# Performance work log

Measured on AMD Instinct MI355X. Metric: run time of the kernel, lower is better.

The kernel has to match this reference:

```python
import jax, jax.numpy as jnp
import numpy as np

B, N, K = 64, 4096, 16
DIN, DOUT, HID, T = 256, 256, 512, 3
LN_EPS = 1e-5


def _ln2d(x, w, b):
    # LayerNorm over last TWO dims (matches nn.LayerNorm([n_feat, dim]))
    m = jnp.mean(x, axis=(-2, -1), keepdims=True)
    v = jnp.mean(jnp.square(x - m), axis=(-2, -1), keepdims=True)
    return (x - m) * jax.lax.rsqrt(v + LN_EPS) * w + b


def setup_inputs() -> dict:
    key = jax.random.key(0)
    ks = jax.random.split(key, 24)
    s = lambda fan_in: 1.0 / np.sqrt(fan_in)
    d = {
        "inputs": jax.random.normal(ks[0], (B, N, DIN), jnp.float32),
        "slots_init": jax.random.normal(ks[1], (B, K, DOUT), jnp.float32),
        "mu": jax.random.normal(ks[2], (1, 1, DOUT), jnp.float32),
        "logsigma": jax.random.normal(ks[3], (1, 1, DOUT), jnp.float32) * 0.1,
        "ln0_w": jnp.ones((N, DIN), jnp.float32),
        "ln0_b": jnp.zeros((N, DIN), jnp.float32),
        "ln1_w": jnp.ones((K, DOUT), jnp.float32),
        "ln1_b": jnp.zeros((K, DOUT), jnp.float32),
        "ln2_w": jnp.ones((K, DOUT), jnp.float32),
        "ln2_b": jnp.zeros((K, DOUT), jnp.float32),
        "qW": jax.random.uniform(ks[4], (T, DOUT, DOUT), jnp.float32, -s(DOUT), s(DOUT)),
        "qb": jax.random.uniform(ks[5], (T, DOUT), jnp.float32, -s(DOUT), s(DOUT)),
        "kW": jax.random.uniform(ks[6], (T, DOUT, DIN), jnp.float32, -s(DIN), s(DIN)),
        "kb": jax.random.uniform(ks[7], (T, DOUT), jnp.float32, -s(DIN), s(DIN)),
        "vW": jax.random.uniform(ks[8], (T, DOUT, DIN), jnp.float32, -s(DIN), s(DIN)),
        "vb": jax.random.uniform(ks[9], (T, DOUT), jnp.float32, -s(DIN), s(DIN)),
        "m1W": jax.random.uniform(ks[10], (T, HID, DOUT), jnp.float32, -s(DOUT), s(DOUT)),
        "m1b": jax.random.uniform(ks[11], (T, HID), jnp.float32, -s(DOUT), s(DOUT)),
        "m2W": jax.random.uniform(ks[12], (T, DOUT, HID), jnp.float32, -s(HID), s(HID)),
        "m2b": jax.random.uniform(ks[13], (T, DOUT), jnp.float32, -s(HID), s(HID)),
    }
    return d


def reference(inputs, slots_init, mu, logsigma, ln0_w, ln0_b, ln1_w, ln1_b,
              ln2_w, ln2_b, qW, qb, kW, kb, vW, vb, m1W, m1b, m2W, m2b):
    slots = mu + jnp.exp(logsigma) * slots_init          # [B,K,DOUT]
    x = _ln2d(inputs, ln0_w, ln0_b)                      # [B,N,DIN]
    for it in range(T):
        s = _ln2d(slots, ln1_w, ln1_b)
        q = jnp.einsum('bkd,ed->bke', s, qW[it]) + qb[it]     # [B,K,DOUT]
        k = jnp.einsum('bnd,ed->bne', x, kW[it]) + kb[it]     # [B,N,DOUT]
        v = jnp.einsum('bnd,ed->bne', x, vW[it]) + vb[it]     # [B,N,DOUT]
        dist = jnp.einsum('bkd,bnd->bkn', q, k) / K           # note: /out_num_features
        attns = jax.nn.softmax(dist, axis=1)                  # softmax over SLOT dim
        weights = attns / (jnp.sum(attns, axis=-1, keepdims=True) + 1e-7)
        slots = jnp.einsum('bkn,bnd->bkd', weights, v)        # [B,K,DOUT]
        h = _ln2d(slots, ln2_w, ln2_b)
        h = jax.nn.relu(jnp.einsum('bkd,hd->bkh', h, m1W[it]) + m1b[it])
        slots = slots + jnp.einsum('bkh,dh->bkd', h, m2W[it]) + m2b[it]
    return slots
```

## Files before the change

kernel.cpp:

```cpp
#include <hip/hip_runtime.h>
#include <hip/hip_bf16.h>

#define LN_EPS 1e-5f

typedef __attribute__((ext_vector_type(8))) short short8;
typedef __attribute__((ext_vector_type(4))) float f32x4;

__device__ __forceinline__ ushort f2bf(float f) {
    __hip_bfloat16 h = __float2bfloat16(f);
    return *reinterpret_cast<ushort*>(&h);
}
__device__ __forceinline__ float bf2f(ushort u) {
    union { float f; unsigned int i; } c; c.i = ((unsigned int)u) << 16; return c.f;
}

__global__ void kprep(const float* __restrict__ qW, const float* __restrict__ kW,
                      const float* __restrict__ m1W, const float* __restrict__ m2W,
                      const float* __restrict__ vW,
                      ushort* __restrict__ qWc, ushort* __restrict__ kWT,
                      ushort* __restrict__ m1Wc, ushort* __restrict__ m2Wc,
                      ushort* __restrict__ vWc,
                      const float* __restrict__ inp, float* __restrict__ sums) {
    __shared__ float tile[64][65];
    __shared__ float r1[256], r2[256];
    int blk = blockIdx.x, t = threadIdx.x;
    if (blk < 288) {
        int col = t & 63, rq = t >> 6;
        const float* src; ushort* dst; int C, tr, tc;
        if (blk < 48)        { int it = blk >> 4, rem = blk & 15; C = 256; tr = rem >> 2; tc = rem & 3;
                               src = qW + it * 65536;  dst = qWc + it * 65536; }
        else if (blk < 96)   { int li = blk - 48; int it = li >> 4, rem = li & 15; C = 256; tr = rem >> 2; tc = rem & 3;
                               src = vW + it * 65536;  dst = vWc + it * 65536; }
        else if (blk < 192)  { int li = blk - 96; int it = li >> 5, rem = li & 31; C = 256; tr = rem >> 2; tc = rem & 3;
                               src = m1W + it * 131072; dst = m1Wc + it * 131072; }
        else                 { int li = blk - 192; int it = li >> 5, rem = li & 31; C = 512; tr = rem >> 3; tc = rem & 7;
                               src = m2W + it * 131072; dst = m2Wc + it * 131072; }
        #pragma unroll
        for (int r = 0; r < 16; r++) {
            int row = r * 4 + rq;
            int idx = (tr * 64 + row) * C + tc * 64 + col;
            dst[idx] = f2bf(src[idx]);
        }
        return;
    }
    if (blk < 336) {
        int col = t & 63, rq = t >> 6;
        int li = blk - 288; int it = li >> 4, rem = li & 15;
        int tr = rem >> 2, tc = rem & 3;
        const float* src = kW + it * 65536; ushort* dst = kWT + it * 65536;
        #pragma unroll
        for (int r = 0; r < 16; r++) {
            int row = r * 4 + rq;
            tile[row][col] = src[(tr * 64 + row) * 256 + tc * 64 + col];
        }
        __syncthreads();
        #pragma unroll
        for (int r = 0; r < 16; r++) {
            int row = r * 4 + rq;
            dst[(tc * 64 + row) * 256 + tr * 64 + col] = f2bf(tile[col][row]);
        }
        return;
    }
    int lb = blk - 336;
    int b = lb >> 5, seg = lb & 31;
    const float4* p = (const float4*)inp + (size_t)b * 262144 + seg * 8192 + t;
    float s = 0.f, sq = 0.f;
    #pragma unroll
    for (int k = 0; k < 32; k++) {
        float4 v = p[k * 256];
        s  += v.x + v.y + v.z + v.w;
        sq += v.x * v.x + v.y * v.y + v.z * v.z + v.w * v.w;
    }
    r1[t] = s; r2[t] = sq; __syncthreads();
    for (int st = 128; st > 0; st >>= 1) {
        if (t < st) { r1[t] += r1[t + st]; r2[t] += r2[t + st]; }
        __syncthreads();
    }
    if (t == 0) { atomicAdd(&sums[b], r1[0]); atomicAdd(&sums[64 + b], r2[0]); }
}

__device__ __forceinline__ void qgen_core(
        int b, int t, int lane, int w, int l15, int quad,
        ushort* slbq, float* qsf, ushort* qsb, ushort* qkl,
        const ushort* __restrict__ qWc, const float* __restrict__ qb,
        const ushort* __restrict__ kWT, const float* __restrict__ kb,
        ushort* __restrict__ qkf, float* __restrict__ qkb,
        float* __restrict__ denom_out) {
    {
        short8 aq[8];
        #pragma unroll
        for (int ds = 0; ds < 8; ds++)
            aq[ds] = *(const short8*)(&slbq[l15 * 264 + ds * 32 + quad * 8]);
        int et = w;
        f32x4 c = f32x4{0.f, 0.f, 0.f, 0.f};
        #pragma unroll
        for (int ds = 0; ds < 8; ds++) {
            short8 bf_ = *(const short8*)(qWc + (size_t)(et * 16 + l15) * 256 + ds * 32 + quad * 8);
            c = __builtin_amdgcn_mfma_f32_16x16x32_bf16(aq[ds], bf_, c, 0, 0, 0);
        }
        float qbv = qb[et * 16 + l15];
        #pragma unroll
        for (int r = 0; r < 4; r++) {
            float val = (c[r] + qbv) * (1.f / 16.f);
            qsf[(quad * 4 + r) * 260 + et * 16 + l15] = val;
            qsb[(quad * 4 + r) * 264 + et * 16 + l15] = f2bf(val);
        }
    }
    __syncthreads();
    {
        float pp = 0.f;
        #pragma unroll
        for (int e = 0; e < 16; e++) pp += qsf[w * 260 + l15 * 16 + e] * kb[l15 * 16 + e];
        pp += __shfl_xor(pp, 1); pp += __shfl_xor(pp, 2);
        pp += __shfl_xor(pp, 4); pp += __shfl_xor(pp, 8);
        if (lane == 0) qkb[b * 16 + w] = pp;
    }
    if (t < 16) denom_out[b * 16 + t] = 0.f;
    {
        short8 aq2[8];
        #pragma unroll
        for (int es = 0; es < 8; es++)
            aq2[es] = *(const short8*)(&qsb[l15 * 264 + es * 32 + quad * 8]);
        int dt = w;
        f32x4 c2 = f32x4{0.f, 0.f, 0.f, 0.f};
        #pragma unroll
        for (int es = 0; es < 8; es++) {
            short8 bf2 = *(const short8*)(kWT + (size_t)(dt * 16 + l15) * 256 + es * 32 + quad * 8);
            c2 = __builtin_amdgcn_mfma_f32_16x16x32_bf16(aq2[es], bf2, c2, 0, 0, 0);
        }
        #pragma unroll
        for (int r = 0; r < 4; r++)
            qkl[(quad * 4 + r) * 264 + dt * 16 + l15] = f2bf(c2[r]);
    }
    __syncthreads();
    if (w < 8) {
        short8 v = *(const short8*)(&qkl[l15 * 264 + w * 32 + quad * 8]);
        *(short8*)(qkf + (size_t)(b * 8 + w) * 512 + lane * 8) = v;
    }
}

__global__ void lkq(const float* __restrict__ inp, const float* __restrict__ ln0w,
                    const float* __restrict__ ln0b, const float* __restrict__ sums,
                    ushort* __restrict__ xgs,
                    const float* __restrict__ slots_init, const float* __restrict__ mu,
                    const float* __restrict__ logsig,
                    const float* __restrict__ ln1w, const float* __restrict__ ln1b,
                    const ushort* __restrict__ qWc, const float* __restrict__ qb,
                    const ushort* __restrict__ kWT, const float* __restrict__ kb,
                    ushort* __restrict__ qkf, float* __restrict__ qkb,
                    float* __restrict__ denom) {
    __shared__ ushort slbq[16 * 264];
    __shared__ ushort qsb[16 * 264];
    __shared__ ushort qkl[16 * 264];
    __shared__ float  qsf[16 * 260];
    __shared__ float  wr1[16], wr2[16];
    int t = threadIdx.x;
    int lane = t & 63, w = t >> 6, l15 = lane & 15, quad = lane >> 4;

    if (blockIdx.x < 256) {
        int gw = blockIdx.x * 16 + w;
        int ntile = gw >> 4;
        int ds = (gw >> 1) & 7;
        int b0 = (gw & 1) * 32;
        int n = ntile * 16 + l15;
        int dcol = ds * 32 + quad * 8;
        const float4* wp = (const float4*)(ln0w + n * 256 + dcol);
        const float4* bp = (const float4*)(ln0b + n * 256 + dcol);
        float4 w0 = wp[0], w1 = wp[1];
        float4 c0 = bp[0], c1 = bp[1];
        #pragma unroll 4
        for (int bi = 0; bi < 32; bi++) {
            int b = b0 + bi;
            float mean = sums[b] * (1.f / 1048576.f);
            float rstd = rsqrtf(sums[64 + b] * (1.f / 1048576.f) - mean * mean + LN_EPS);
            const float4* xp = (const float4*)(inp + (size_t)b * 1048576 + n * 256 + dcol);
            float4 v0 = xp[0], v1 = xp[1];
            ushort o[8];
            o[0] = f2bf((v0.x - mean) * rstd * w0.x + c0.x);
            o[1] = f2bf((v0.y - mean) * rstd * w0.y + c0.y);
            o[2] = f2bf((v0.z - mean) * rstd * w0.z + c0.z);
            o[3] = f2bf((v0.w - mean) * rstd * w0.w + c0.w);
            o[4] = f2bf((v1.x - mean) * rstd * w1.x + c1.x);
            o[5] = f2bf((v1.y - mean) * rstd * w1.y + c1.y);
            o[6] = f2bf((v1.z - mean) * rstd * w1.z + c1.z);
            o[7] = f2bf((v1.w - mean) * rstd * w1.w + c1.w);
            *(short8*)(xgs + ((size_t)((b * 256 + ntile) * 8 + ds) * 64 + lane) * 8) = *(short8*)o;
        }
        return;
    }
    int b = blockIdx.x - 256;
    int g = t >> 8, c = t & 255;
    float muv = mu[c];
    float sgv = __expf(logsig[c]);
    float vals[4]; float s = 0.f, sq = 0.f;
    #pragma unroll
    for (int kk = 0; kk < 4; kk++) {
        float v = muv + sgv * slots_init[b * 4096 + (g * 4 + kk) * 256 + c];
        vals[kk] = v; s += v; sq += v * v;
    }
    #pragma unroll
    for (int m = 1; m < 64; m <<= 1) { s += __shfl_xor(s, m); sq += __shfl_xor(sq, m); }
    if (lane == 0) { wr1[w] = s; wr2[w] = sq; }
    __syncthreads();
    float ts = 0.f, tsq = 0.f;
    #pragma unroll
    for (int i = 0; i < 16; i++) { ts += wr1[i]; tsq += wr2[i]; }
    float m_  = ts * (1.f / 4096.f);
    float rs_ = rsqrtf(tsq * (1.f / 4096.f) - m_ * m_ + LN_EPS);
    #pragma unroll
    for (int kk = 0; kk < 4; kk++) {
        int k = g * 4 + kk;
        slbq[k * 264 + c] = f2bf((vals[kk] - m_) * rs_ * ln1w[k * 256 + c] + ln1b[k * 256 + c]);
    }
    __syncthreads();
    qgen_core(b, t, lane, w, l15, quad, slbq, qsf, qsb, qkl,
              qWc, qb, kWT, kb, qkf, qkb, denom);
}

__launch_bounds__(256, 4)
__global__ void katt(const ushort* __restrict__ xgs, const ushort* __restrict__ qkf,
                     const float* __restrict__ qkb, float* __restrict__ denom,
                     float* __restrict__ partials) {
    int b = blockIdx.x >> 4, chunk = blockIdx.x & 15;
    int tid = threadIdx.x;
    int lane = tid & 63, w = tid >> 6;
    int l15 = lane & 15, quad = lane >> 4;

    __shared__ ushort xtT[16384];
    __shared__ ushort attn[16 * 72];

    short8 ilo, ihi;
    #pragma unroll
    for (int j = 0; j < 8; j++) {
        ilo[j] = (short)((quad * 8 + j == l15)      ? 0x3F80 : 0);
        ihi[j] = (short)((quad * 8 + j == l15 + 16) ? 0x3F80 : 0);
    }
    int wbase = (w >> 1) * 512 + ((w * 2 + (quad >> 1)) & 3) * 128 + l15 * 8 + (quad & 1) * 4;

    short8 qkfr[8];
    #pragma unroll
    for (int ds = 0; ds < 8; ds++)
        qkfr[ds] = *(const short8*)(qkf + ((size_t)(b * 8 + ds) * 512 + lane * 8));
    float4 qo = *(const float4*)(qkb + b * 16 + quad * 4);

    f32x4 pacc[4];
    #pragma unroll
    for (int u = 0; u < 4; u++) pacc[u] = f32x4{0.f, 0.f, 0.f, 0.f};
    float dp0 = 0.f, dp1 = 0.f, dp2 = 0.f, dp3 = 0.f;

    int tile0 = b * 256 + chunk * 16;

    short8 pf[8];
    #pragma unroll
    for (int i = 0; i < 8; i++)
        pf[i] = *(const short8*)(xgs + (((size_t)(tile0 + w) * 8 + i) * 64 + lane) * 8);

    #pragma unroll 1
    for (int sub = 0; sub < 4; sub++) {
        __syncthreads();
        f32x4 dc = f32x4{0.f, 0.f, 0.f, 0.f};
        #pragma unroll
        for (int ds = 0; ds < 8; ds++)
            dc = __builtin_amdgcn_mfma_f32_16x16x32_bf16(qkfr[ds], pf[ds], dc, 0, 0, 0);
        dc[0] += qo.x; dc[1] += qo.y; dc[2] += qo.z; dc[3] += qo.w;
        float mx = fmaxf(fmaxf(dc[0], dc[1]), fmaxf(dc[2], dc[3]));
        mx = fmaxf(mx, __shfl_xor(mx, 16));
        mx = fmaxf(mx, __shfl_xor(mx, 32));
        float e0 = __expf(dc[0] - mx), e1 = __expf(dc[1] - mx);
        float e2 = __expf(dc[2] - mx), e3 = __expf(dc[3] - mx);
        float lsum = e0 + e1 + e2 + e3;
        lsum += __shfl_xor(lsum, 16); lsum += __shfl_xor(lsum, 32);
        float inv = 1.f / lsum;
        float p0 = e0 * inv, p1 = e1 * inv, p2 = e2 * inv, p3 = e3 * inv;
        dp0 += p0; dp1 += p1; dp2 += p2; dp3 += p3;
        attn[(quad * 4 + 0) * 72 + w * 16 + l15] = f2bf(p0);
        attn[(quad * 4 + 1) * 72 + w * 16 + l15] = f2bf(p1);
        attn[(quad * 4 + 2) * 72 + w * 16 + l15] = f2bf(p2);
        attn[(quad * 4 + 3) * 72 + w * 16 + l15] = f2bf(p3);
        f32x4 zz = f32x4{0.f, 0.f, 0.f, 0.f};
        #pragma unroll
        for (int ds = 0; ds < 8; ds++) {
            f32x4 tlo = __builtin_amdgcn_mfma_f32_16x16x32_bf16(pf[ds], ilo, zz, 0, 0, 0);
            f32x4 thi = __builtin_amdgcn_mfma_f32_16x16x32_bf16(pf[ds], ihi, zz, 0, 0, 0);
            unsigned lo0 = (__float_as_uint(tlo[0]) >> 16) | (__float_as_uint(tlo[1]) & 0xFFFF0000u);
            unsigned lo1 = (__float_as_uint(tlo[2]) >> 16) | (__float_as_uint(tlo[3]) & 0xFFFF0000u);
            unsigned hi0 = (__float_as_uint(thi[0]) >> 16) | (__float_as_uint(thi[1]) & 0xFFFF0000u);
            unsigned hi1 = (__float_as_uint(thi[2]) >> 16) | (__float_as_uint(thi[3]) & 0xFFFF0000u);
            *(uint2*)(&xtT[(ds * 2 + 0) * 1024 + wbase]) = make_uint2(lo0, lo1);
            *(uint2*)(&xtT[(ds * 2 + 1) * 1024 + wbase]) = make_uint2(hi0, hi1);
        }
        if (sub < 3) {
            #pragma unroll
            for (int i = 0; i < 8; i++)
                pf[i] = *(const short8*)(xgs + (((size_t)(tile0 + (sub + 1) * 4 + w) * 8 + i) * 64 + lane) * 8);
        }
        __syncthreads();

        #pragma unroll
        for (int ns = 0; ns < 2; ns++) {
            short8 aa = *(const short8*)(&attn[l15 * 72 + ns * 32 + quad * 8]);
            #pragma unroll
            for (int u = 0; u < 4; u++) {
                short8 bb = *(const short8*)(&xtT[((w * 4 + u) * 2 + ns) * 512 + lane * 8]);
                pacc[u] = __builtin_amdgcn_mfma_f32_16x16x32_bf16(aa, bb, pacc[u], 0, 0, 0);
            }
        }
    }

    #pragma unroll
    for (int m = 1; m < 16; m <<= 1) {
        dp0 += __shfl_xor(dp0, m); dp1 += __shfl_xor(dp1, m);
        dp2 += __shfl_xor(dp2, m); dp3 += __shfl_xor(dp3, m);
    }
    if (l15 == 0) {
        atomicAdd(&denom[b * 16 + quad * 4 + 0], dp0);
        atomicAdd(&denom[b * 16 + quad * 4 + 1], dp1);
        atomicAdd(&denom[b * 16 + quad * 4 + 2], dp2);
        atomicAdd(&denom[b * 16 + quad * 4 + 3], dp3);
    }

    float* pout = partials + (size_t)(b * 16 + chunk) * 4096;
    #pragma unroll
    for (int u = 0; u < 4; u++)
        #pragma unroll
        for (int r = 0; r < 4; r++)
            pout[(quad * 4 + r) * 256 + (w * 4 + u) * 16 + l15] = pacc[u][r];
}

__global__ void ktail(const float* __restrict__ partials, const float* __restrict__ denom,
                      const ushort* __restrict__ vWc, const float* __restrict__ vb,
                      const float* __restrict__ ln2w, const float* __restrict__ ln2b,
                      const ushort* __restrict__ m1Wc, const float* __restrict__ m1b,
                      const ushort* __restrict__ m2Wc, const float* __restrict__ m2b,
                      float* __restrict__ final_out, int write_final,
                      const float* __restrict__ ln1w, const float* __restrict__ ln1b,
                      const ushort* __restrict__ qWc_n, const float* __restrict__ qb_n,
                      const ushort* __restrict__ kWT_n, const float* __restrict__ kb_n,
                      ushort* __restrict__ qkf, float* __restrict__ qkb,
                      float* __restrict__ denom_out, int gen) {
    int b = blockIdx.x, t = threadIdx.x;
    int lane = t & 63, w = t >> 6, l15 = lane & 15, quad = lane >> 4;

    __shared__ char pool[60416];
    __shared__ float dnb[16];
    __shared__ float wr1[16], wr2[16];
    ushort* axsb = (ushort*)pool;
    ushort* s2b  = (ushort*)(pool + 8448);
    float*  slt  = (float*)(pool + 16896);
    ushort* hlb  = (ushort*)(pool + 35328);
    float*  slt2 = (float*)pool;
    ushort* slbq = (ushort*)(pool + 16896);
    ushort* qkl  = (ushort*)(pool + 16896);
    float*  qsf  = (float*)(pool + 35328);
    ushort* qsb  = (ushort*)(pool + 51968);

    const float* pp = partials + (size_t)b * 65536;
    #pragma unroll
    for (int i = 0; i < 4; i++) {
        int idx = i * 1024 + t;
        float ss = 0.f;
        #pragma unroll
        for (int c = 0; c < 16; c++) ss += pp[c * 4096 + idx];
        axsb[(idx >> 8) * 264 + (idx & 255)] = f2bf(ss);
    }
    if (t < 16) dnb[t] = denom[b * 16 + t];
    __syncthreads();

    float myv[4];
    {
        short8 af[8];
        #pragma unroll
        for (int ds = 0; ds < 8; ds++)
            af[ds] = *(const short8*)(&axsb[l15 * 264 + ds * 32 + quad * 8]);
        int et = w;
        f32x4 c = f32x4{0.f, 0.f, 0.f, 0.f};
        #pragma unroll
        for (int ds = 0; ds < 8; ds++) {
            short8 bf_ = *(const short8*)(vWc + (size_t)(et * 16 + l15) * 256 + ds * 32 + quad * 8);
            c = __builtin_amdgcn_mfma_f32_16x16x32_bf16(af[ds], bf_, c, 0, 0, 0);
        }
        float vbe = vb[et * 16 + l15];
        #pragma unroll
        for (int r = 0; r < 4; r++) {
            float A = dnb[quad * 4 + r];
            float val = (c[r] + vbe * A) / (A + 1e-7f);
            slt[(quad * 4 + r) * 256 + et * 16 + l15] = val;
            myv[r] = val;
        }
    }
    {
        float s = myv[0] + myv[1] + myv[2] + myv[3];
        float sq = myv[0]*myv[0] + myv[1]*myv[1] + myv[2]*myv[2] + myv[3]*myv[3];
        #pragma unroll
        for (int m = 1; m < 64; m <<= 1) { s += __shfl_xor(s, m); sq += __shfl_xor(sq, m); }
        if (lane == 0) { wr1[w] = s; wr2[w] = sq; }
        __syncthreads();
    }
    float ts = 0.f, tsq = 0.f;
    #pragma unroll
    for (int i = 0; i < 16; i++) { ts += wr1[i]; tsq += wr2[i]; }
    float m2_ = ts * (1.f / 4096.f);
    float rs2 = rsqrtf(tsq * (1.f / 4096.f) - m2_ * m2_ + LN_EPS);
    {
        int e = w * 16 + l15;
        #pragma unroll
        for (int r = 0; r < 4; r++) {
            int ss_ = quad * 4 + r;
            s2b[ss_ * 264 + e] = f2bf((myv[r] - m2_) * rs2 * ln2w[ss_ * 256 + e] + ln2b[ss_ * 256 + e]);
        }
    }
    __syncthreads();

    {
        short8 a2[8];
        #pragma unroll
        for (int ds = 0; ds < 8; ds++)
            a2[ds] = *(const short8*)(&s2b[l15 * 264 + ds * 32 + quad * 8]);
        #pragma unroll
        for (int p = 0; p < 2; p++) {
            int jt = w + p * 16;
            f32x4 c = f32x4{0.f, 0.f, 0.f, 0.f};
            #pragma unroll
            for (int ds = 0; ds < 8; ds++) {
                short8 bf_ = *(const short8*)(m1Wc + (size_t)(jt * 16 + l15) * 256 + ds * 32 + quad * 8);
                c = __builtin_amdgcn_mfma_f32_16x16x32_bf16(a2[ds], bf_, c, 0, 0, 0);
            }
            float bias = m1b[jt * 16 + l15];
            #pragma unroll
            for (int r = 0; r < 4; r++)
                hlb[(quad * 4 + r) * 520 + jt * 16 + l15] = f2bf(fmaxf(c[r] + bias, 0.f));
        }
    }
    __syncthreads();

    {
        short8 a3[16];
        #pragma unroll
        for (int js = 0; js < 16; js++)
            a3[js] = *(const short8*)(&hlb[l15 * 520 + js * 32 + quad * 8]);
        int dt = w;
        f32x4 c = f32x4{0.f, 0.f, 0.f, 0.f};
        #pragma unroll
        for (int js = 0; js < 16; js++) {
            short8 bf_ = *(const short8*)(m2Wc + (size_t)(dt * 16 + l15) * 512 + js * 32 + quad * 8);
            c = __builtin_amdgcn_mfma_f32_16x16x32_bf16(a3[js], bf_, c, 0, 0, 0);
        }
        float b2 = m2b[dt * 16 + l15];
        #pragma unroll
        for (int r = 0; r < 4; r++) {
            int ss_ = quad * 4 + r, d = dt * 16 + l15;
            float val = slt[ss_ * 256 + d] + c[r] + b2;
            slt2[ss_ * 256 + d] = val;
            if (write_final) final_out[(size_t)b * 4096 + ss_ * 256 + d] = val;
        }
    }
    __syncthreads();

    if (gen) {
        int g = t >> 8, cc = t & 255;
        float vals[4]; float s = 0.f, sq = 0.f;
        #pragma unroll
        for (int kk = 0; kk < 4; kk++) {
            float v = slt2[(g * 4 + kk) * 256 + cc];
            vals[kk] = v; s += v; sq += v * v;
        }
        #pragma unroll
        for (int m = 1; m < 64; m <<= 1) { s += __shfl_xor(s, m); sq += __shfl_xor(sq, m); }
        if (lane == 0) { wr1[w] = s; wr2[w] = sq; }
        __syncthreads();
        float ts1 = 0.f, tsq1 = 0.f;
        #pragma unroll
        for (int i = 0; i < 16; i++) { ts1 += wr1[i]; tsq1 += wr2[i]; }
        float m1_ = ts1 * (1.f / 4096.f);
        float rs1 = rsqrtf(tsq1 * (1.f / 4096.f) - m1_ * m1_ + LN_EPS);
        #pragma unroll
        for (int kk = 0; kk < 4; kk++) {
            int k = g * 4 + kk;
            slbq[k * 264 + cc] = f2bf((vals[kk] - m1_) * rs1 * ln1w[k * 256 + cc] + ln1b[k * 256 + cc]);
        }
        __syncthreads();
        qgen_core(b, t, lane, w, l15, quad, slbq, qsf, qsb, qkl,
                  qWc_n, qb_n, kWT_n, kb_n, qkf, qkb, denom_out);
    }
}

extern "C" void kernel_launch(void* const* d_in, const int* in_sizes, int n_in,
                              void* d_out, int out_size, void* d_ws, size_t ws_size,
                              hipStream_t stream) {
    const float* inputs     = (const float*)d_in[0];
    const float* slots_init = (const float*)d_in[1];
    const float* mu         = (const float*)d_in[2];
    const float* logsig     = (const float*)d_in[3];
    const float* ln0w       = (const float*)d_in[4];
    const float* ln0b       = (const float*)d_in[5];
    const float* ln1w       = (const float*)d_in[6];
    const float* ln1b       = (const float*)d_in[7];
    const float* ln2w       = (const float*)d_in[8];
    const float* ln2b       = (const float*)d_in[9];
    const float* qW         = (const float*)d_in[10];
    const float* qb         = (const float*)d_in[11];
    const float* kW         = (const float*)d_in[12];
    const float* kb         = (const float*)d_in[13];
    const float* vW         = (const float*)d_in[14];
    const float* vb         = (const float*)d_in[15];
    const float* m1W        = (const float*)d_in[16];
    const float* m1b        = (const float*)d_in[17];
    const float* m2W        = (const float*)d_in[18];
    const float* m2b        = (const float*)d_in[19];

    char* ws = (char*)d_ws;
    ushort* xgs     = (ushort*)(ws);
    float*  partials= (float*)(ws + 134217728);
    ushort* qkf     = (ushort*)(ws + 150994944);
    ushort* qWc     = (ushort*)(ws + 153616384);
    ushort* m1Wc    = (ushort*)(ws + 154009600);
    ushort* m2Wc    = (ushort*)(ws + 154796032);
    ushort* vWc     = (ushort*)(ws + 155582464);
    float*  denom   = (float*)(ws + 155975680);
    float*  qkb     = (float*)(ws + 155979776);
    float*  sums    = (float*)(ws + 155983872);
    ushort* kWT     = (ushort*)(ws + 155984384);

    hipMemsetAsync(sums, 0, 512, stream);
    kprep<<<2384, 256, 0, stream>>>(qW, kW, m1W, m2W, vW, qWc, kWT, m1Wc, m2Wc, vWc,
                                    inputs, sums);
    lkq<<<320, 1024, 0, stream>>>(inputs, ln0w, ln0b, sums, xgs,
                                  slots_init, mu, logsig, ln1w, ln1b,
                                  qWc, qb, kWT, kb, qkf, qkb, denom);

    for (int it = 0; it < 3; it++) {
        katt<<<1024, 256, 0, stream>>>(xgs, qkf, qkb, denom, partials);
        int nx = (it < 2) ? it + 1 : 2;
        ktail<<<64, 1024, 0, stream>>>(partials, denom,
                                       vWc + it * 65536, vb + it * 256, ln2w, ln2b,
                                       m1Wc + it * 131072, m1b + it * 512,
                                       m2Wc + it * 131072, m2b + it * 256,
                                       (float*)d_out, it == 2 ? 1 : 0,
                                       ln1w, ln1b,
                                       qWc + nx * 65536, qb + nx * 256,
                                       kWT + nx * 65536, kb + nx * 256,
                                       qkf, qkb, denom, it < 2 ? 1 : 0);
    }
}
```

Before: 316.9 us.

## Fuse tail into attention kernel via last-block-per-batch atomic counter

Removes the separate ktail launch by having each attention block increment a per-batch counter. The last of the 16 chunk blocks for a batch then runs the tail work: reduce the partials, apply the V projection, LayerNorm, the MLP, and generate the next iteration's q/k. This cuts a kernel launch and its grid-wide barrier per iteration. The cost is that the tail now runs on only 256 threads instead of 1024 and adds threadfence/atomic overhead, so the last block per batch can lengthen the critical path.

```diff
diff --git a/kernel.cpp b/kernel.cpp
--- a/kernel.cpp
+++ b/kernel.cpp
@@ -218,16 +218,28 @@
 }
 
 __launch_bounds__(256, 4)
-__global__ void katt(const ushort* __restrict__ xgs, const ushort* __restrict__ qkf,
-                     const float* __restrict__ qkb, float* __restrict__ denom,
-                     float* __restrict__ partials) {
+__global__ void katta(const ushort* __restrict__ xgs, ushort* __restrict__ qkf,
+                      float* __restrict__ qkb, float* __restrict__ denom,
+                      float* __restrict__ partials, int* __restrict__ cnt,
+                      const ushort* __restrict__ vWc, const float* __restrict__ vb,
+                      const float* __restrict__ ln2w, const float* __restrict__ ln2b,
+                      const ushort* __restrict__ m1Wc, const float* __restrict__ m1b,
+                      const ushort* __restrict__ m2Wc, const float* __restrict__ m2b,
+                      float* __restrict__ final_out, int write_final,
+                      const float* __restrict__ ln1w, const float* __restrict__ ln1b,
+                      const ushort* __restrict__ qWc_n, const float* __restrict__ qb_n,
+                      const ushort* __restrict__ kWT_n, const float* __restrict__ kb_n,
+                      int gen) {
     int b = blockIdx.x >> 4, chunk = blockIdx.x & 15;
     int tid = threadIdx.x;
     int lane = tid & 63, w = tid >> 6;
     int l15 = lane & 15, quad = lane >> 4;
 
-    __shared__ ushort xtT[16384];
-    __shared__ ushort attn[16 * 72];
+    __shared__ char pool[35712];
+    __shared__ float dnb[16];
+    __shared__ int isLast;
+    ushort* xtT  = (ushort*)pool;
+    ushort* attn = (ushort*)(pool + 32768);
 
     short8 ilo, ihi;
     #pragma unroll
@@ -325,88 +337,77 @@
         #pragma unroll
         for (int r = 0; r < 4; r++)
             pout[(quad * 4 + r) * 256 + (w * 4 + u) * 16 + l15] = pacc[u][r];
-}
-
-__global__ void ktail(const float* __restrict__ partials, const float* __restrict__ denom,
-                      const ushort* __restrict__ vWc, const float* __restrict__ vb,
-                      const float* __restrict__ ln2w, const float* __restrict__ ln2b,
-                      const ushort* __restrict__ m1Wc, const float* __restrict__ m1b,
-                      const ushort* __restrict__ m2Wc, const float* __restrict__ m2b,
-                      float* __restrict__ final_out, int write_final,
-                      const float* __restrict__ ln1w, const float* __restrict__ ln1b,
-                      const ushort* __restrict__ qWc_n, const float* __restrict__ qb_n,
-                      const ushort* __restrict__ kWT_n, const float* __restrict__ kb_n,
-                      ushort* __restrict__ qkf, float* __restrict__ qkb,
-                      float* __restrict__ denom_out, int gen) {
-    int b = blockIdx.x, t = threadIdx.x;
-    int lane = t & 63, w = t >> 6, l15 = lane & 15, quad = lane >> 4;
-
-    __shared__ char pool[60416];
-    __shared__ float dnb[16];
-    __shared__ float wr1[16], wr2[16];
+
+    __threadfence();
+    __syncthreads();
+    if (tid == 0) { int old = atomicAdd(cnt + b, 1); isLast = (old == 15); }
+    __syncthreads();
+    if (!isLast) return;
+    __threadfence();
+
     ushort* axsb = (ushort*)pool;
     ushort* s2b  = (ushort*)(pool + 8448);
-    float*  slt  = (float*)(pool + 16896);
-    ushort* hlb  = (ushort*)(pool + 35328);
-    float*  slt2 = (float*)pool;
-    ushort* slbq = (ushort*)(pool + 16896);
-    ushort* qkl  = (ushort*)(pool + 16896);
-    float*  qsf  = (float*)(pool + 35328);
-    ushort* qsb  = (ushort*)(pool + 51968);
+    ushort* hlb  = (ushort*)(pool + 16896);
+    float*  r1   = (float*)(pool + 33536);
+    float*  r2   = (float*)(pool + 34560);
+    ushort* slbq = (ushort*)pool;
+    ushort* qklp = (ushort*)pool;
+    ushort* qsb  = (ushort*)(pool + 8448);
+    float*  qsf  = (float*)(pool + 16896);
 
     const float* pp = partials + (size_t)b * 65536;
     #pragma unroll
-    for (int i = 0; i < 4; i++) {
-        int idx = i * 1024 + t;
+    for (int i = 0; i < 16; i++) {
         float ss = 0.f;
         #pragma unroll
-        for (int c = 0; c < 16; c++) ss += pp[c * 4096 + idx];
-        axsb[(idx >> 8) * 264 + (idx & 255)] = f2bf(ss);
-    }
-    if (t < 16) dnb[t] = denom[b * 16 + t];
-    __syncthreads();
-
-    float myv[4];
+        for (int c = 0; c < 16; c++) ss += pp[c * 4096 + i * 256 + tid];
+        axsb[i * 264 + tid] = f2bf(ss);
+    }
+    if (tid < 16) dnb[tid] = denom[b * 16 + tid];
+    __syncthreads();
+
+    float myv[16];
     {
         short8 af[8];
         #pragma unroll
         for (int ds = 0; ds < 8; ds++)
             af[ds] = *(const short8*)(&axsb[l15 * 264 + ds * 32 + quad * 8]);
-        int et = w;
-        f32x4 c = f32x4{0.f, 0.f, 0.f, 0.f};
-        #pragma unroll
-        for (int ds = 0; ds < 8; ds++) {
-            short8 bf_ = *(const short8*)(vWc + (size_t)(et * 16 + l15) * 256 + ds * 32 + quad * 8);
-            c = __builtin_amdgcn_mfma_f32_16x16x32_bf16(af[ds], bf_, c, 0, 0, 0);
-        }
-        float vbe = vb[et * 16 + l15];
-        #pragma unroll
-        for (int r = 0; r < 4; r++) {
-            float A = dnb[quad * 4 + r];
-            float val = (c[r] + vbe * A) / (A + 1e-7f);
-            slt[(quad * 4 + r) * 256 + et * 16 + l15] = val;
-            myv[r] = val;
+        #pragma unroll
+        for (int u = 0; u < 4; u++) {
+            int et = w * 4 + u;
+            f32x4 c = f32x4{0.f, 0.f, 0.f, 0.f};
+            #pragma unroll
+            for (int ds = 0; ds < 8; ds++) {
+                short8 bf_ = *(const short8*)(vWc + (size_t)(et * 16 + l15) * 256 + ds * 32 + quad * 8);
+                c = __builtin_amdgcn_mfma_f32_16x16x32_bf16(af[ds], bf_, c, 0, 0, 0);
+            }
+            float vbe = vb[et * 16 + l15];
+            #pragma unroll
+            for (int r = 0; r < 4; r++) {
+                float A = dnb[quad * 4 + r];
+                myv[u * 4 + r] = (c[r] + vbe * A) / (A + 1e-7f);
+            }
         }
     }
     {
-        float s = myv[0] + myv[1] + myv[2] + myv[3];
-        float sq = myv[0]*myv[0] + myv[1]*myv[1] + myv[2]*myv[2] + myv[3]*myv[3];
-        #pragma unroll
-        for (int m = 1; m < 64; m <<= 1) { s += __shfl_xor(s, m); sq += __shfl_xor(sq, m); }
-        if (lane == 0) { wr1[w] = s; wr2[w] = sq; }
-        __syncthreads();
-    }
-    float ts = 0.f, tsq = 0.f;
-    #pragma unroll
-    for (int i = 0; i < 16; i++) { ts += wr1[i]; tsq += wr2[i]; }
-    float m2_ = ts * (1.f / 4096.f);
-    float rs2 = rsqrtf(tsq * (1.f / 4096.f) - m2_ * m2_ + LN_EPS);
-    {
-        int e = w * 16 + l15;
+        float s = 0.f, sq = 0.f;
+        #pragma unroll
+        for (int i = 0; i < 16; i++) { s += myv[i]; sq += myv[i] * myv[i]; }
+        r1[tid] = s; r2[tid] = sq; __syncthreads();
+        for (int st = 128; st > 0; st >>= 1) {
+            if (tid < st) { r1[tid] += r1[tid + st]; r2[tid] += r2[tid + st]; }
+            __syncthreads();
+        }
+    }
+    float m2_ = r1[0] * (1.f / 4096.f);
+    float rs2 = rsqrtf(r2[0] * (1.f / 4096.f) - m2_ * m2_ + LN_EPS);
+    #pragma unroll
+    for (int u = 0; u < 4; u++) {
+        int e = (w * 4 + u) * 16 + l15;
         #pragma unroll
         for (int r = 0; r < 4; r++) {
             int ss_ = quad * 4 + r;
-            s2b[ss_ * 264 + e] = f2bf((myv[r] - m2_) * rs2 * ln2w[ss_ * 256 + e] + ln2b[ss_ * 256 + e]);
+            s2b[ss_ * 264 + e] = f2bf((myv[u * 4 + r] - m2_) * rs2 * ln2w[ss_ * 256 + e] + ln2b[ss_ * 256 + e]);
         }
     }
     __syncthreads();
@@ -417,8 +418,8 @@
         for (int ds = 0; ds < 8; ds++)
             a2[ds] = *(const short8*)(&s2b[l15 * 264 + ds * 32 + quad * 8]);
         #pragma unroll
-        for (int p = 0; p < 2; p++) {
-            int jt = w + p * 16;
+        for (int p = 0; p < 8; p++) {
+            int jt = w * 8 + p;
             f32x4 c = f32x4{0.f, 0.f, 0.f, 0.f};
             #pragma unroll
             for (int ds = 0; ds < 8; ds++) {
@@ -433,54 +434,119 @@
     }
     __syncthreads();
 
-    {
-        short8 a3[16];
-        #pragma unroll
-        for (int js = 0; js < 16; js++)
-            a3[js] = *(const short8*)(&hlb[l15 * 520 + js * 32 + quad * 8]);
-        int dt = w;
-        f32x4 c = f32x4{0.f, 0.f, 0.f, 0.f};
-        #pragma unroll
-        for (int js = 0; js < 16; js++) {
-            short8 bf_ = *(const short8*)(m2Wc + (size_t)(dt * 16 + l15) * 512 + js * 32 + quad * 8);
-            c = __builtin_amdgcn_mfma_f32_16x16x32_bf16(a3[js], bf_, c, 0, 0, 0);
-        }
-        float b2 = m2b[dt * 16 + l15];
+    f32x4 cacc[4];
+    #pragma unroll
+    for (int u = 0; u < 4; u++) cacc[u] = f32x4{0.f, 0.f, 0.f, 0.f};
+    #pragma unroll
+    for (int half = 0; half < 2; half++) {
+        short8 a3[8];
+        #pragma unroll
+        for (int j8 = 0; j8 < 8; j8++)
+            a3[j8] = *(const short8*)(&hlb[l15 * 520 + (half * 8 + j8) * 32 + quad * 8]);
+        #pragma unroll
+        for (int u = 0; u < 4; u++) {
+            int dt = w * 4 + u;
+            #pragma unroll
+            for (int j8 = 0; j8 < 8; j8++) {
+                short8 bf_ = *(const short8*)(m2Wc + (size_t)(dt * 16 + l15) * 512 + (half * 8 + j8) * 32 + quad * 8);
+                cacc[u] = __builtin_amdgcn_mfma_f32_16x16x32_bf16(a3[j8], bf_, cacc[u], 0, 0, 0);
+            }
+        }
+    }
+    float nv[16];
+    float sn = 0.f, sqn = 0.f;
+    #pragma unroll
+    for (int u = 0; u < 4; u++) {
+        int d = (w * 4 + u) * 16 + l15;
+        float b2 = m2b[d];
         #pragma unroll
         for (int r = 0; r < 4; r++) {
-            int ss_ = quad * 4 + r, d = dt * 16 + l15;
-            float val = slt[ss_ * 256 + d] + c[r] + b2;
-            slt2[ss_ * 256 + d] = val;
+            int ss_ = quad * 4 + r;
+            float val = myv[u * 4 + r] + cacc[u][r] + b2;
+            nv[u * 4 + r] = val;
             if (write_final) final_out[(size_t)b * 4096 + ss_ * 256 + d] = val;
-        }
-    }
-    __syncthreads();
+            sn += val; sqn += val * val;
+        }
+    }
 
     if (gen) {
-        int g = t >> 8, cc = t & 255;
-        float vals[4]; float s = 0.f, sq = 0.f;
-        #pragma unroll
-        for (int kk = 0; kk < 4; kk++) {
-            float v = slt2[(g * 4 + kk) * 256 + cc];
-            vals[kk] = v; s += v; sq += v * v;
-        }
-        #pragma unroll
-        for (int m = 1; m < 64; m <<= 1) { s += __shfl_xor(s, m); sq += __shfl_xor(sq, m); }
-        if (lane == 0) { wr1[w] = s; wr2[w] = sq; }
+        r1[tid] = sn; r2[tid] = sqn; __syncthreads();
+        for (int st = 128; st > 0; st >>= 1) {
+            if (tid < st) { r1[tid] += r1[tid + st]; r2[tid] += r2[tid + st]; }
+            __syncthreads();
+        }
+        float m1_ = r1[0] * (1.f / 4096.f);
+        float rs1 = rsqrtf(r2[0] * (1.f / 4096.f) - m1_ * m1_ + LN_EPS);
+        #pragma unroll
+        for (int u = 0; u < 4; u++) {
+            int d = (w * 4 + u) * 16 + l15;
+            #pragma unroll
+            for (int r = 0; r < 4; r++) {
+                int ss_ = quad * 4 + r;
+                slbq[ss_ * 264 + d] = f2bf((nv[u * 4 + r] - m1_) * rs1 * ln1w[ss_ * 256 + d] + ln1b[ss_ * 256 + d]);
+            }
+        }
         __syncthreads();
-        float ts1 = 0.f, tsq1 = 0.f;
-        #pragma unroll
-        for (int i = 0; i < 16; i++) { ts1 += wr1[i]; tsq1 += wr2[i]; }
-        float m1_ = ts1 * (1.f / 4096.f);
-        float rs1 = rsqrtf(tsq1 * (1.f / 4096.f) - m1_ * m1_ + LN_EPS);
-        #pragma unroll
-        for (int kk = 0; kk < 4; kk++) {
-            int k = g * 4 + kk;
-            slbq[k * 264 + cc] = f2bf((vals[kk] - m1_) * rs1 * ln1w[k * 256 + cc] + ln1b[k * 256 + cc]);
+        {
+            short8 aq[8];
+            #pragma unroll
+            for (int ds = 0; ds < 8; ds++)
+                aq[ds] = *(const short8*)(&slbq[l15 * 264 + ds * 32 + quad * 8]);
+            #pragma unroll
+            for (int p = 0; p < 4; p++) {
+                int et = w * 4 + p;
+                f32x4 c = f32x4{0.f, 0.f, 0.f, 0.f};
+                #pragma unroll
+                for (int ds = 0; ds < 8; ds++) {
+                    short8 bf_ = *(const short8*)(qWc_n + (size_t)(et * 16 + l15) * 256 + ds * 32 + quad * 8);
+                    c = __builtin_amdgcn_mfma_f32_16x16x32_bf16(aq[ds], bf_, c, 0, 0, 0);
+                }
+                float qbv = qb_n[et * 16 + l15];
+                #pragma unroll
+                for (int r = 0; r < 4; r++) {
+                    float val = (c[r] + qbv) * (1.f / 16.f);
+                    qsf[(quad * 4 + r) * 260 + et * 16 + l15] = val;
+                    qsb[(quad * 4 + r) * 264 + et * 16 + l15] = f2bf(val);
+                }
+            }
         }
         __syncthreads();
-        qgen_core(b, t, lane, w, l15, quad, slbq, qsf, qsb, qkl,
-                  qWc_n, qb_n, kWT_n, kb_n, qkf, qkb, denom_out);
+        {
+            int ss = w * 4 + quad;
+            float pp2 = 0.f;
+            #pragma unroll
+            for (int e = 0; e < 16; e++) pp2 += qsf[ss * 260 + l15 * 16 + e] * kb_n[l15 * 16 + e];
+            pp2 += __shfl_xor(pp2, 1); pp2 += __shfl_xor(pp2, 2);
+            pp2 += __shfl_xor(pp2, 4); pp2 += __shfl_xor(pp2, 8);
+            if (l15 == 0) qkb[b * 16 + ss] = pp2;
+        }
+        if (tid < 16) denom[b * 16 + tid] = 0.f;
+        {
+            short8 aq2[8];
+            #pragma unroll
+            for (int es = 0; es < 8; es++)
+                aq2[es] = *(const short8*)(&qsb[l15 * 264 + es * 32 + quad * 8]);
+            #pragma unroll
+            for (int p = 0; p < 4; p++) {
+                int dt = w * 4 + p;
+                f32x4 c2 = f32x4{0.f, 0.f, 0.f, 0.f};
+                #pragma unroll
+                for (int es = 0; es < 8; es++) {
+                    short8 bf2 = *(const short8*)(kWT_n + (size_t)(dt * 16 + l15) * 256 + es * 32 + quad * 8);
+                    c2 = __builtin_amdgcn_mfma_f32_16x16x32_bf16(aq2[es], bf2, c2, 0, 0, 0);
+                }
+                #pragma unroll
+                for (int r = 0; r < 4; r++)
+                    qklp[(quad * 4 + r) * 264 + dt * 16 + l15] = f2bf(c2[r]);
+            }
+        }
+        __syncthreads();
+        #pragma unroll
+        for (int i = 0; i < 2; i++) {
+            int ds = w * 2 + i;
+            short8 v = *(const short8*)(&qklp[l15 * 264 + ds * 32 + quad * 8]);
+            *(short8*)(qkf + (size_t)(b * 8 + ds) * 512 + lane * 8) = v;
+        }
     }
 }
 
@@ -520,8 +586,10 @@
     float*  qkb     = (float*)(ws + 155979776);
     float*  sums    = (float*)(ws + 155983872);
     ushort* kWT     = (ushort*)(ws + 155984384);
+    int*    cnt     = (int*)(ws + 156377600);
 
     hipMemsetAsync(sums, 0, 512, stream);
+    hipMemsetAsync(cnt, 0, 768, stream);
     kprep<<<2384, 256, 0, stream>>>(qW, kW, m1W, m2W, vW, qWc, kWT, m1Wc, m2Wc, vWc,
                                     inputs, sums);
     lkq<<<320, 1024, 0, stream>>>(inputs, ln0w, ln0b, sums, xgs,
@@ -529,16 +597,15 @@
                                   qWc, qb, kWT, kb, qkf, qkb, denom);
 
     for (int it = 0; it < 3; it++) {
-        katt<<<1024, 256, 0, stream>>>(xgs, qkf, qkb, denom, partials);
         int nx = (it < 2) ? it + 1 : 2;
-        ktail<<<64, 1024, 0, stream>>>(partials, denom,
-                                       vWc + it * 65536, vb + it * 256, ln2w, ln2b,
-                                       m1Wc + it * 131072, m1b + it * 512,
-                                       m2Wc + it * 131072, m2b + it * 256,
-                                       (float*)d_out, it == 2 ? 1 : 0,
-                                       ln1w, ln1b,
-                                       qWc + nx * 65536, qb + nx * 256,
-                                       kWT + nx * 65536, kb + nx * 256,
-                                       qkf, qkb, denom, it < 2 ? 1 : 0);
+        katta<<<1024, 256, 0, stream>>>(xgs, qkf, qkb, denom, partials, cnt + it * 64,
+                                        vWc + it * 65536, vb + it * 256, ln2w, ln2b,
+                                        m1Wc + it * 131072, m1b + it * 512,
+                                        m2Wc + it * 131072, m2b + it * 256,
+                                        (float*)d_out, it == 2 ? 1 : 0,
+                                        ln1w, ln1b,
+                                        qWc + nx * 65536, qb + nx * 256,
+                                        kWT + nx * 65536, kb + nx * 256,
+                                        it < 2 ? 1 : 0);
     }
 }
```

Result: slower. 1.110 ms (+250.2%).
